# Performance work log

Measured on AMD Instinct MI355X. Metric: run time of the kernel, lower is better.

Reference implementation:

```python
import jax, jax.numpy as jnp
import numpy as np

INPUT, HIDDEN = 15, 20

def setup_inputs() -> dict:
    key = jax.random.key(0)
    k1, k2, k3, k4, k5 = jax.random.split(key, 5)
    B, T = 4096, 512
    s = 1.0 / np.sqrt(HIDDEN)  # torch default uniform init bound
    feature = jax.random.normal(k1, (B, T, INPUT), dtype=jnp.float32)
    W_ih = jax.random.uniform(k2, (HIDDEN, INPUT), jnp.float32, -s, s)
    W_hh = jax.random.uniform(k3, (HIDDEN, HIDDEN), jnp.float32, -s, s)
    b_ih = jax.random.uniform(k4, (HIDDEN,), jnp.float32, -s, s)
    b_hh = jax.random.uniform(k5, (HIDDEN,), jnp.float32, -s, s)
    return {"feature": feature, "W_ih": W_ih, "W_hh": W_hh, "b_ih": b_ih, "b_hh": b_hh}

def reference(feature, W_ih, W_hh, b_ih, b_hh):
    # h_t = tanh(x_t @ W_ih^T + b_ih + h_{t-1} @ W_hh^T + b_hh)
    B, T, _ = feature.shape
    # precompute input projections for all timesteps: [T, B, H]
    xp = jnp.einsum('bti,hi->tbh', feature, W_ih) + (b_ih + b_hh)
    h0 = jnp.zeros((B, HIDDEN), dtype=feature.dtype)
    def step(h, x_t):
        h_new = jnp.tanh(x_t + h @ W_hh.T)
        return h_new, None
    hn, _ = jax.lax.scan(step, h0, xp)
    return hn  # [B, H] == hn.squeeze() for num_layers=1
```

## Files before the change

### kernel.cpp

```cpp
#include <hip/hip_runtime.h>
#include <cstddef>


typedef float g4 __attribute__((ext_vector_type(4), aligned(4)));
typedef float g2 __attribute__((ext_vector_type(2), aligned(4)));
typedef _Float16 h2  __attribute__((ext_vector_type(2)));
typedef _Float16 v8h __attribute__((ext_vector_type(8)));
typedef _Float16 v4h __attribute__((ext_vector_type(4)));

#define TT 512
#define IN 15
#define HD 20
#define CH 32
#define NCH (TT / CH)
#define XROW 16
#define XGRP (CH * XROW + 16)
#define XBUF (3 * XGRP)
#define HROW 24

#define P2(v, i) __builtin_shufflevector(v, v, 2 * (i), 2 * (i) + 1)
#define FD(acc, p, w) acc = __builtin_amdgcn_fdot2(p, w, acc, false)

__global__ __launch_bounds__(64) void rnn_fused(
    const float* __restrict__ feature, const float* __restrict__ W_ih,
    const float* __restrict__ W_hh, const float* __restrict__ b_ih,
    const float* __restrict__ b_hh, float* __restrict__ out, int B) {
  __shared__ __align__(16) _Float16 xh[2 * XBUF];
  __shared__ __align__(16) _Float16 hh[4 * HROW];

  const int lane = threadIdx.x;
  const int g = lane / HD;
  const int j = lane - g * HD;
  const int gx = (g < 3) ? g : 2;
  const int bid = blockIdx.x;
  const int b = bid * 3 + g;

  if (lane < 48) ((float*)hh)[lane] = 0.f;

  h2 wih[8];
  {
    const float* wr = W_ih + j * IN;
#pragma unroll
    for (int i = 0; i < 7; ++i)
      wih[i] = (h2){(_Float16)wr[2 * i], (_Float16)wr[2 * i + 1]};
    wih[7] = (h2){(_Float16)wr[14], (_Float16)0.f};
  }
  h2 whh[10];
  {
    const float* wr = W_hh + j * HD;
#pragma unroll
    for (int i = 0; i < 10; ++i)
      whh[i] = (h2){(_Float16)wr[2 * i], (_Float16)wr[2 * i + 1]};
  }
  const float bias = b_ih[j] + b_hh[j];

  const int grA = lane >> 5;
  const int tcA = lane & 31;
  const int bc = B - 1;
  const int bA = min(bid * 3 + grA, bc);
  const int bB = min(bid * 3 + 2, bc);
  const float* baseA = feature + ((size_t)bA * TT + tcA) * IN;
  const float* baseB = feature + ((size_t)bB * TT + tcA) * IN;

  g4 rA0, rA1, rA2; g2 rA3; float rA4;
  g4 rB0, rB1, rB2; g2 rB3; float rB4;

  auto issue = [&](int t0) {
    const float* s = baseA + (size_t)t0 * IN;
    rA0 = *(const g4*)(s);      rA1 = *(const g4*)(s + 4);
    rA2 = *(const g4*)(s + 8);  rA3 = *(const g2*)(s + 12);
    rA4 = s[14];
    if (lane < 32) {
      const float* s2 = baseB + (size_t)t0 * IN;
      rB0 = *(const g4*)(s2);     rB1 = *(const g4*)(s2 + 4);
      rB2 = *(const g4*)(s2 + 8); rB3 = *(const g2*)(s2 + 12);
      rB4 = s2[14];
    }
  };
  auto commit = [&](int bsel) {
    v8h lo = {(_Float16)rA0.x, (_Float16)rA0.y, (_Float16)rA0.z, (_Float16)rA0.w,
              (_Float16)rA1.x, (_Float16)rA1.y, (_Float16)rA1.z, (_Float16)rA1.w};
    v8h hi = {(_Float16)rA2.x, (_Float16)rA2.y, (_Float16)rA2.z, (_Float16)rA2.w,
              (_Float16)rA3.x, (_Float16)rA3.y, (_Float16)rA4,   (_Float16)0.f};
    _Float16* d = xh + bsel * XBUF + grA * XGRP + tcA * XROW;
    *(v8h*)d = lo; *((v8h*)d + 1) = hi;
    if (lane < 32) {
      v8h lo2 = {(_Float16)rB0.x, (_Float16)rB0.y, (_Float16)rB0.z, (_Float16)rB0.w,
                 (_Float16)rB1.x, (_Float16)rB1.y, (_Float16)rB1.z, (_Float16)rB1.w};
      v8h hi2 = {(_Float16)rB2.x, (_Float16)rB2.y, (_Float16)rB2.z, (_Float16)rB2.w,
                 (_Float16)rB3.x, (_Float16)rB3.y, (_Float16)rB4,   (_Float16)0.f};
      _Float16* d2 = xh + bsel * XBUF + 2 * XGRP + tcA * XROW;
      *(v8h*)d2 = lo2; *((v8h*)d2 + 1) = hi2;
    }
  };

  issue(0);
  commit(0);

  float hn = 0.f;
  const _Float16* hrd = hh + g * HROW;
  _Float16* hwr = hh + g * HROW + j;
  for (int c = 0; c < NCH; ++c) {
    if (c + 1 < NCH) issue((c + 1) * CH);
    const _Float16* xg = xh + (c & 1) * XBUF + gx * XGRP;
#pragma unroll 4
    for (int tc = 0; tc < CH; ++tc) {
      v8h ha = *(const v8h*)hrd;
      v8h hb = *(const v8h*)(hrd + 8);
      v4h hc = *(const v4h*)(hrd + 16);
      const v8h* xp = (const v8h*)(xg + tc * XROW);
      v8h xa = xp[0], xb = xp[1];
      float a0 = bias, a1 = 0.f, a2 = 0.f, a3 = 0.f;
      FD(a0, P2(xa, 0), wih[0]); FD(a1, P2(xa, 1), wih[1]);
      FD(a2, P2(xa, 2), wih[2]); FD(a3, P2(xa, 3), wih[3]);
      FD(a0, P2(xb, 0), wih[4]); FD(a1, P2(xb, 1), wih[5]);
      FD(a2, P2(xb, 2), wih[6]); FD(a3, P2(xb, 3), wih[7]);
      FD(a0, P2(ha, 0), whh[0]); FD(a1, P2(ha, 1), whh[1]);
      FD(a2, P2(ha, 2), whh[2]); FD(a3, P2(ha, 3), whh[3]);
      FD(a0, P2(hb, 0), whh[4]); FD(a1, P2(hb, 1), whh[5]);
      FD(a2, P2(hb, 2), whh[6]); FD(a3, P2(hb, 3), whh[7]);
      FD(a0, P2(hc, 0), whh[8]); FD(a1, P2(hc, 1), whh[9]);
      float s = (a0 + a1) + (a2 + a3);
      float e = exp2f(s * 2.8853900817779268f);
      hn = 1.f - 2.f * __builtin_amdgcn_rcpf(1.f + e);
      *hwr = (_Float16)hn;
    }
    if (c + 1 < NCH) commit((c + 1) & 1);
  }
  if (g < 3 && b < B) out[(size_t)b * HD + j] = hn;
}

extern "C" void kernel_launch(void* const* d_in, const int* in_sizes, int n_in,
                              void* d_out, int out_size, void* d_ws, size_t ws_size,
                              hipStream_t stream) {
  const float* feature = (const float*)d_in[0];
  const float* W_ih    = (const float*)d_in[1];
  const float* W_hh    = (const float*)d_in[2];
  const float* b_ih    = (const float*)d_in[3];
  const float* b_hh    = (const float*)d_in[4];
  float* out = (float*)d_out;
  const int B = in_sizes[0] / (TT * IN);
  const int grid = (B + 2) / 3;
  rnn_fused<<<grid, 64, 0, stream>>>(feature, W_ih, W_hh, b_ih, b_hh, out, B);
}
```

Before: 232.3 us.

## Pipeline LDS reads of h and x, fold tanh scale into weights, swizzle x rows

Restructures the recurrent step so the next step's hidden-state and input rows are read from LDS right after the current step's h write, keeping the values in registers across iterations. The 2/ln2 exponent scale is pre-multiplied into the weights and bias, which removes one multiply per step. Input rows in shared memory are XOR-swizzled to reduce bank conflicts on the packed stores and loads. The h buffer is no longer zeroed, since the initial h now lives in registers. Rounding the scaled weights to fp16 changes numerics slightly, and the cross-lane ordering of the h write and the next read within a wave rests on wave-synchronous execution with no barrier.

```diff
diff --git a/kernel.cpp b/kernel.cpp
--- a/kernel.cpp
+++ b/kernel.cpp
@@ -21,6 +21,8 @@
 #define P2(v, i) __builtin_shufflevector(v, v, 2 * (i), 2 * (i) + 1)
 #define FD(acc, p, w) acc = __builtin_amdgcn_fdot2(p, w, acc, false)
 
+__device__ __forceinline__ int xsw(int r) { return (r << 4) ^ ((r & 4) << 1); }
+
 __global__ __launch_bounds__(64) void rnn_fused(
     const float* __restrict__ feature, const float* __restrict__ W_ih,
     const float* __restrict__ W_hh, const float* __restrict__ b_ih,
@@ -35,24 +37,24 @@
   const int bid = blockIdx.x;
   const int b = bid * 3 + g;
 
-  if (lane < 48) ((float*)hh)[lane] = 0.f;
+  const float K = 2.8853900817779268f;
 
   h2 wih[8];
   {
     const float* wr = W_ih + j * IN;
 #pragma unroll
     for (int i = 0; i < 7; ++i)
-      wih[i] = (h2){(_Float16)wr[2 * i], (_Float16)wr[2 * i + 1]};
-    wih[7] = (h2){(_Float16)wr[14], (_Float16)0.f};
+      wih[i] = (h2){(_Float16)(K * wr[2 * i]), (_Float16)(K * wr[2 * i + 1])};
+    wih[7] = (h2){(_Float16)(K * wr[14]), (_Float16)0.f};
   }
   h2 whh[10];
   {
     const float* wr = W_hh + j * HD;
 #pragma unroll
     for (int i = 0; i < 10; ++i)
-      whh[i] = (h2){(_Float16)wr[2 * i], (_Float16)wr[2 * i + 1]};
+      whh[i] = (h2){(_Float16)(K * wr[2 * i]), (_Float16)(K * wr[2 * i + 1])};
   }
-  const float bias = b_ih[j] + b_hh[j];
+  const float bias = K * (b_ih[j] + b_hh[j]);
 
   const int grA = lane >> 5;
   const int tcA = lane & 31;
@@ -82,14 +84,14 @@
               (_Float16)rA1.x, (_Float16)rA1.y, (_Float16)rA1.z, (_Float16)rA1.w};
     v8h hi = {(_Float16)rA2.x, (_Float16)rA2.y, (_Float16)rA2.z, (_Float16)rA2.w,
               (_Float16)rA3.x, (_Float16)rA3.y, (_Float16)rA4,   (_Float16)0.f};
-    _Float16* d = xh + bsel * XBUF + grA * XGRP + tcA * XROW;
+    _Float16* d = xh + bsel * XBUF + grA * XGRP + xsw(tcA);
     *(v8h*)d = lo; *((v8h*)d + 1) = hi;
     if (lane < 32) {
       v8h lo2 = {(_Float16)rB0.x, (_Float16)rB0.y, (_Float16)rB0.z, (_Float16)rB0.w,
                  (_Float16)rB1.x, (_Float16)rB1.y, (_Float16)rB1.z, (_Float16)rB1.w};
       v8h hi2 = {(_Float16)rB2.x, (_Float16)rB2.y, (_Float16)rB2.z, (_Float16)rB2.w,
                  (_Float16)rB3.x, (_Float16)rB3.y, (_Float16)rB4,   (_Float16)0.f};
-      _Float16* d2 = xh + bsel * XBUF + 2 * XGRP + tcA * XROW;
+      _Float16* d2 = xh + bsel * XBUF + 2 * XGRP + xsw(tcA);
       *(v8h*)d2 = lo2; *((v8h*)d2 + 1) = hi2;
     }
   };
@@ -97,35 +99,58 @@
   issue(0);
   commit(0);
 
+  v8h xa, xb;
+  {
+    const v8h* xp = (const v8h*)(xh + gx * XGRP + xsw(0));
+    xa = xp[0]; xb = xp[1];
+  }
+
+  v8h ha, hb; v4h hc;
+#pragma unroll
+  for (int i = 0; i < 8; ++i) { ha[i] = (_Float16)0.f; hb[i] = (_Float16)0.f; }
+#pragma unroll
+  for (int i = 0; i < 4; ++i) hc[i] = (_Float16)0.f;
+
   float hn = 0.f;
   const _Float16* hrd = hh + g * HROW;
   _Float16* hwr = hh + g * HROW + j;
+
+  auto step = [&](const _Float16* xg, int tcn) {
+    float a0 = bias, a1 = 0.f, a2 = 0.f, a3 = 0.f;
+    FD(a0, P2(xa, 0), wih[0]); FD(a1, P2(xa, 1), wih[1]);
+    FD(a2, P2(xa, 2), wih[2]); FD(a3, P2(xa, 3), wih[3]);
+    FD(a0, P2(xb, 0), wih[4]); FD(a1, P2(xb, 1), wih[5]);
+    FD(a2, P2(xb, 2), wih[6]); FD(a3, P2(xb, 3), wih[7]);
+    FD(a0, P2(ha, 0), whh[0]); FD(a1, P2(ha, 1), whh[1]);
+    FD(a2, P2(ha, 2), whh[2]); FD(a3, P2(ha, 3), whh[3]);
+    FD(a0, P2(hb, 0), whh[4]); FD(a1, P2(hb, 1), whh[5]);
+    FD(a2, P2(hb, 2), whh[6]); FD(a3, P2(hb, 3), whh[7]);
+    FD(a0, P2(hc, 0), whh[8]); FD(a1, P2(hc, 1), whh[9]);
+    float s = (a0 + a1) + (a2 + a3);
+    float e = exp2f(s);
+    hn = 1.f - 2.f * __builtin_amdgcn_rcpf(1.f + e);
+    *hwr = (_Float16)hn;
+    ha = *(const v8h*)hrd;
+    hb = *(const v8h*)(hrd + 8);
+    hc = *(const v4h*)(hrd + 16);
+    if (tcn >= 0) {
+      const v8h* xp = (const v8h*)(xg + xsw(tcn));
+      xa = xp[0]; xb = xp[1];
+    }
+  };
+
   for (int c = 0; c < NCH; ++c) {
     if (c + 1 < NCH) issue((c + 1) * CH);
     const _Float16* xg = xh + (c & 1) * XBUF + gx * XGRP;
 #pragma unroll 4
-    for (int tc = 0; tc < CH; ++tc) {
-      v8h ha = *(const v8h*)hrd;
-      v8h hb = *(const v8h*)(hrd + 8);
-      v4h hc = *(const v4h*)(hrd + 16);
-      const v8h* xp = (const v8h*)(xg + tc * XROW);
-      v8h xa = xp[0], xb = xp[1];
-      float a0 = bias, a1 = 0.f, a2 = 0.f, a3 = 0.f;
-      FD(a0, P2(xa, 0), wih[0]); FD(a1, P2(xa, 1), wih[1]);
-      FD(a2, P2(xa, 2), wih[2]); FD(a3, P2(xa, 3), wih[3]);
-      FD(a0, P2(xb, 0), wih[4]); FD(a1, P2(xb, 1), wih[5]);
-      FD(a2, P2(xb, 2), wih[6]); FD(a3, P2(xb, 3), wih[7]);
-      FD(a0, P2(ha, 0), whh[0]); FD(a1, P2(ha, 1), whh[1]);
-      FD(a2, P2(ha, 2), whh[2]); FD(a3, P2(ha, 3), whh[3]);
-      FD(a0, P2(hb, 0), whh[4]); FD(a1, P2(hb, 1), whh[5]);
-      FD(a2, P2(hb, 2), whh[6]); FD(a3, P2(hb, 3), whh[7]);
-      FD(a0, P2(hc, 0), whh[8]); FD(a1, P2(hc, 1), whh[9]);
-      float s = (a0 + a1) + (a2 + a3);
-      float e = exp2f(s * 2.8853900817779268f);
-      hn = 1.f - 2.f * __builtin_amdgcn_rcpf(1.f + e);
-      *hwr = (_Float16)hn;
+    for (int tc = 0; tc < CH - 1; ++tc) step(xg, tc + 1);
+    step(xg, -1);
+    if (c + 1 < NCH) {
+      commit((c + 1) & 1);
+      const v8h* xp =
+          (const v8h*)(xh + ((c + 1) & 1) * XBUF + gx * XGRP + xsw(0));
+      xa = xp[0]; xb = xp[1];
     }
-    if (c + 1 < NCH) commit((c + 1) & 1);
   }
   if (g < 3 && b < B) out[(size_t)b * HD + j] = hn;
 }
```

Result: no change. 232.1 us (-0.1%).
